# Kernel optimization log

Measured on AMD Instinct MI355X. Metric: run time of the kernel, lower is better.

Reference implementation:

```python
import jax, jax.numpy as jnp
import numpy as np
jax.config.update("jax_enable_x64", True)

N = 16384   # nodes
C = 16      # initial color vocabulary size
B = 64      # number of graphs in the batch
_rs = np.random.RandomState(42)
_MULTS = jnp.asarray((_rs.randint(1, 2 ** 62, size=C + 1).astype(np.int64) << 1) | 1)  # odd 64-bit hash multipliers


def setup_inputs() -> dict:
    key = jax.random.key(0)
    k1, k2, k3 = jax.random.split(key, 3)
    x = jax.random.randint(k1, (N,), 0, C, dtype=jnp.int64)
    adj_t = jax.random.randint(k2, (N, N), 0, 2).astype(jnp.float32)  # dense binary adjacency
    batch = jnp.sort(jax.random.randint(k3, (N,), 0, B, dtype=jnp.int64))
    return {"x": x, "adj_t": adj_t, "batch": batch}


def _wl_colors(x, adj_t):
    # One WL refinement step. The torch code hashes (own_color, sorted neighbor colors)
    # and assigns new ids by insertion order into an OrderedDict ('isolate' -> 0).
    # A sorted tuple of neighbor colors is equivalent to the neighbor color multiset,
    # which we represent as a count histogram and hash with a 64-bit wraparound
    # polynomial hash; ids are then assigned by first-occurrence (node-index) order.
    n = x.shape[0]
    onehot = jax.nn.one_hot(x, C, dtype=adj_t.dtype)                 # [N, C]
    nbr_hist = jnp.round(adj_t @ onehot).astype(jnp.int64)           # [N, C] neighbor color counts
    iso = (adj_t.sum(axis=1) + adj_t.sum(axis=0)) == 0               # isolated nodes
    h = x * _MULTS[0] + (nbr_hist * _MULTS[1:]).sum(axis=-1)         # int64 wraparound hash
    h = jnp.where(iso, jnp.int64(-(2 ** 63)), h)
    order = jnp.argsort(h)
    hs = h[order]
    new_grp = jnp.concatenate([jnp.ones((1,), bool), hs[1:] != hs[:-1]])
    gid = jnp.zeros(n, jnp.int64).at[order].set(jnp.cumsum(new_grp) - 1)   # group id per node
    first_of_grp = jax.ops.segment_min(jnp.arange(n), gid, num_segments=n)
    firsts = first_of_grp[gid]                                       # first node index with same signature
    is_first = (~iso) & (firsts == jnp.arange(n))
    rank = jnp.cumsum(is_first.astype(jnp.int64))                    # hashmap insertion order (1-based)
    return jnp.where(iso, 0, rank[firsts])                           # 'isolate' -> 0


def _histogram(colors, batch):
    # Per-graph color histogram; width padded to N+1 (max possible distinct colors)
    # for static shapes -- extra columns are zero and do not affect the L2 norm.
    num_colors = N + 1
    idx = batch * num_colors + colors
    out = jnp.zeros(B * num_colors, jnp.int64).at[idx].add(1)
    out = out.reshape(B, num_colors)[:, 1:]                          # drop 'isolate' column
    out = out.astype(jnp.float64)
    return out / jnp.linalg.norm(out, axis=-1, keepdims=True)


def reference(x, adj_t, batch):
    colors = _wl_colors(x, adj_t)          # forward's default return value
    hist = _histogram(colors, batch)       # return_embedding=True output
    return hist, colors
```

## Files before the change

### kernel.cpp

```cpp
#include <hip/hip_runtime.h>
#include <stdint.h>

#define NN 16384
#define NC 16
#define NB 64

#define HSIZE 65536
#define HMASK 65535
#define HSENT 0xFFFFFFFFFFFFFFFFull
#define HGOLD 0x9E3779B97F4A7C15ull

typedef unsigned int vuint4 __attribute__((ext_vector_type(4)));

struct Mults { unsigned long long m[17]; };

__device__ __forceinline__ void htab_insert(unsigned long long* __restrict__ hk,
                                            int* __restrict__ hv,
                                            unsigned long long key, int idx) {
  if (key == HSENT) key -= 1;
  unsigned slot = (unsigned)((key * HGOLD) >> 48);
  for (;;) {
    unsigned long long old = atomicCAS(&hk[slot], HSENT, key);
    if (old == HSENT || old == key) { atomicMin(&hv[slot], idx); return; }
    slot = (slot + 1) & HMASK;
  }
}


__global__ __launch_bounds__(256) void k_init(const int* __restrict__ x,
                                              unsigned long long* __restrict__ table,
                                              int* __restrict__ scount,
                                              int* __restrict__ cnt,
                                              unsigned long long* __restrict__ hk,
                                              int* __restrict__ hv) {
  int idx = blockIdx.x * 256 + threadIdx.x;
  if (idx == 0) *scount = 0;
  if (idx < 4096) {
    int c = idx & 15, k = (idx >> 4) & 3, chunk = idx >> 6;
    unsigned long long m = 0ull;
    for (int l = 0; l < 64; ++l) {
      int col = chunk * 256 + l * 4 + k;
      if (x[col] == c) m |= (1ull << l);
    }
    table[idx] = m;
  }
  hk[idx] = HSENT;
  hv[idx] = 0x7fffffff;
  int4 z = {0, 0, 0, 0};
  int4* c4 = (int4*)cnt;
  #pragma unroll
  for (int r = 0; r < 4; ++r) c4[(size_t)idx * 4 + r] = z;
}

__global__ __launch_bounds__(256) void k_hist(const float* __restrict__ adj,
                                              const unsigned long long* __restrict__ table,
                                              const int* __restrict__ x,
                                              Mults M,
                                              unsigned long long* __restrict__ h,
                                              int* __restrict__ iso,
                                              int* __restrict__ suspects,
                                              int* __restrict__ scount,
                                              unsigned long long* __restrict__ hk,
                                              int* __restrict__ hv) {
  int wave = threadIdx.x >> 6;
  int lane = threadIdx.x & 63;
  int row  = blockIdx.x * 4 + wave;
  int xv   = x[row];
  const vuint4* rowp = (const vuint4*)(adj + (size_t)row * NN);
  int c = lane & 15;
  int k = lane >> 4;
  const unsigned long long* tk = table + (k * 16 + c);
  int cnt = 0;
  #pragma unroll 4
  for (int chunk = 0; chunk < 64; ++chunk) {
    vuint4 v = __builtin_nontemporal_load(&rowp[chunk * 64 + lane]);
    unsigned long long tm = tk[chunk * 64];
    unsigned long long b0 = __ballot(v.x != 0u);
    unsigned long long b1 = __ballot(v.y != 0u);
    unsigned long long b2 = __ballot(v.z != 0u);
    unsigned long long b3 = __ballot(v.w != 0u);
    unsigned long long m = (k & 2) ? ((k & 1) ? b3 : b2) : ((k & 1) ? b1 : b0);
    cnt += __popcll(m & tm);
  }
  cnt += __shfl_xor(cnt, 16, 64);
  cnt += __shfl_xor(cnt, 32, 64);
  int rs = cnt;
  rs += __shfl_xor(rs, 1, 64);
  rs += __shfl_xor(rs, 2, 64);
  rs += __shfl_xor(rs, 4, 64);
  rs += __shfl_xor(rs, 8, 64);
  unsigned long long hl = (unsigned long long)(long long)cnt * M.m[(lane & 15) + 1];
  hl += __shfl_xor(hl, 1, 64);
  hl += __shfl_xor(hl, 2, 64);
  hl += __shfl_xor(hl, 4, 64);
  hl += __shfl_xor(hl, 8, 64);
  if (lane == 0) {
    unsigned long long hf = hl + (unsigned long long)(long long)xv * M.m[0];
    h[row] = hf;
    if (rs == 0) {
      int s = atomicAdd(scount, 1);
      suspects[s] = row;
    } else {
      htab_insert(hk, hv, hf, row);
    }
  }
  if (lane == 1) iso[row] = 0;
}

__global__ __launch_bounds__(256) void k_colcheck(const float* __restrict__ adj,
                                                  const int* __restrict__ suspects,
                                                  const int* __restrict__ scount,
                                                  int* __restrict__ iso,
                                                  const unsigned long long* __restrict__ h,
                                                  unsigned long long* __restrict__ hk,
                                                  int* __restrict__ hv) {
  __shared__ int red[256];
  int nsus = *scount;
  for (int u = blockIdx.x; u < nsus; u += gridDim.x) {
    int col = suspects[u];
    int any = 0;
    for (int r = threadIdx.x; r < NN; r += 256)
      any |= (adj[(size_t)r * NN + col] != 0.0f);
    red[threadIdx.x] = any;
    __syncthreads();
    for (int s = 128; s > 0; s >>= 1) {
      if (threadIdx.x < s) red[threadIdx.x] |= red[threadIdx.x + s];
      __syncthreads();
    }
    if (threadIdx.x == 0) {
      if (red[0] == 0) iso[col] = 1;
      else             htab_insert(hk, hv, h[col], col);
    }
    __syncthreads();
  }
}

__global__ __launch_bounds__(256) void k_lookup(const int* __restrict__ iso,
                                                const unsigned long long* __restrict__ h,
                                                const unsigned long long* __restrict__ hk,
                                                const int* __restrict__ hv,
                                                int* __restrict__ firsts) {
  int i = blockIdx.x * 256 + threadIdx.x;
  int f = -1;
  if (!iso[i]) {
    unsigned long long key = h[i];
    if (key == HSENT) key -= 1;
    unsigned slot = (unsigned)((key * HGOLD) >> 48);
    unsigned long long kk = hk[slot];
    while (kk != key) { slot = (slot + 1) & HMASK; kk = hk[slot]; }
    f = hv[slot];
  }
  firsts[i] = f;
}

__global__ __launch_bounds__(1024) void k_scan(const int* __restrict__ firsts,
                                               const int* __restrict__ batch,
                                               float* __restrict__ out_colors,
                                               int* __restrict__ cnt) {
  __shared__ int rank_lds[NN];
  __shared__ int wsum[16];
  int t = threadIdx.x;
  int lane = t & 63, wv = t >> 6;
  int base = t * 16;
  int fidx[16];
  int loc[16];
  int s = 0;
  #pragma unroll
  for (int u = 0; u < 16; ++u) {
    int i = base + u;
    int f = firsts[i];
    fidx[u] = f;
    int isf = (f == i);
    s += isf;
    loc[u] = s;
  }
  int incl = s;
  #pragma unroll
  for (int off = 1; off < 64; off <<= 1) {
    int v = __shfl_up(incl, off, 64);
    if (lane >= off) incl += v;
  }
  if (lane == 63) wsum[wv] = incl;
  __syncthreads();
  if (t == 0) {
    int acc = 0;
    #pragma unroll
    for (int w = 0; w < 16; ++w) { int v = wsum[w]; wsum[w] = acc; acc += v; }
  }
  __syncthreads();
  int excl = wsum[wv] + incl - s;
  #pragma unroll
  for (int u = 0; u < 16; ++u) rank_lds[base + u] = excl + loc[u];
  __syncthreads();
  #pragma unroll
  for (int u = 0; u < 16; ++u) {
    int i = base + u;
    int c = (fidx[u] < 0) ? 0 : rank_lds[fidx[u]];
    out_colors[i] = (float)c;
    if (c > 0) atomicAdd(&cnt[(size_t)batch[i] * NN + (c - 1)], 1);
  }
}

__global__ __launch_bounds__(256) void k_norm(const int* __restrict__ cnt,
                                              float* __restrict__ out) {
  __shared__ float red[256];
  int b = blockIdx.x;
  const int4* c4 = (const int4*)(cnt + (size_t)b * NN);
  float4* o4 = (float4*)(out + (size_t)b * NN);
  float ss = 0.0f;
  for (int j = threadIdx.x; j < NN / 4; j += 256) {
    int4 v = c4[j];
    float4 f = {(float)v.x, (float)v.y, (float)v.z, (float)v.w};
    ss += f.x * f.x + f.y * f.y + f.z * f.z + f.w * f.w;
  }
  red[threadIdx.x] = ss;
  __syncthreads();
  for (int s = 128; s > 0; s >>= 1) {
    if (threadIdx.x < s) red[threadIdx.x] += red[threadIdx.x + s];
    __syncthreads();
  }
  float inv = 1.0f / sqrtf(red[0]);
  for (int j = threadIdx.x; j < NN / 4; j += 256) {
    int4 v = c4[j];
    float4 f = {(float)v.x * inv, (float)v.y * inv, (float)v.z * inv, (float)v.w * inv};
    o4[j] = f;
  }
}


struct MTState { uint32_t mt[624]; int idx; };

static void mt_seed(MTState& s, uint32_t seed) {
  s.mt[0] = seed;
  for (int i = 1; i < 624; ++i)
    s.mt[i] = 1812433253u * (s.mt[i - 1] ^ (s.mt[i - 1] >> 30)) + (uint32_t)i;
  s.idx = 624;
}

static uint32_t mt_next(MTState& s) {
  if (s.idx >= 624) {
    for (int i = 0; i < 624; ++i) {
      uint32_t y = (s.mt[i] & 0x80000000u) | (s.mt[(i + 1) % 624] & 0x7fffffffu);
      uint32_t nx = s.mt[(i + 397) % 624] ^ (y >> 1);
      if (y & 1u) nx ^= 2567483615u;
      s.mt[i] = nx;
    }
    s.idx = 0;
  }
  uint32_t y = s.mt[s.idx++];
  y ^= y >> 11;
  y ^= (y << 7) & 2636928640u;
  y ^= (y << 15) & 4022730752u;
  y ^= y >> 18;
  return y;
}

static uint64_t mt_next64(MTState& s) {
  uint64_t hi = mt_next(s);
  uint64_t lo = mt_next(s);
  return (hi << 32) | lo;
}


extern "C" void kernel_launch(void* const* d_in, const int* in_sizes, int n_in,
                              void* d_out, int out_size, void* d_ws, size_t ws_size,
                              hipStream_t stream) {
  const int*   x     = (const int*)d_in[0];
  const float* adj   = (const float*)d_in[1];
  const int*   batch = (const int*)d_in[2];
  float* out_hist   = (float*)d_out;
  float* out_colors = out_hist + (size_t)NB * NN;

  char* ws = (char*)d_ws;
  int*                cnt      = (int*)(ws + 0);
  int*                scount   = (int*)(ws + 4194304);
  int*                suspects = (int*)(ws + 4194560);
  unsigned long long* h        = (unsigned long long*)(ws + 4260096);
  int*                iso      = (int*)(ws + 4391168);
  int*                firsts   = (int*)(ws + 4456704);
  unsigned long long* table    = (unsigned long long*)(ws + 4522240);
  unsigned long long* hk       = (unsigned long long*)(ws + 4554752);
  int*                hv       = (int*)(ws + 5079040);

  Mults M;
  {
    MTState st;
    mt_seed(st, 42u);
    const uint64_t mask62 = (1ull << 62) - 1ull;
    const uint64_t rng    = (1ull << 62) - 2ull;
    for (int i = 0; i < 17; ++i) {
      uint64_t v;
      do { v = mt_next64(st) & mask62; } while (v > rng);
      M.m[i] = ((1ull + v) << 1) | 1ull;
    }
  }

  k_init<<<256, 256, 0, stream>>>(x, table, scount, cnt, hk, hv);
  k_hist<<<NN / 4, 256, 0, stream>>>(adj, table, x, M, h, iso, suspects, scount, hk, hv);
  k_colcheck<<<64, 256, 0, stream>>>(adj, suspects, scount, iso, h, hk, hv);
  k_lookup<<<NN / 256, 256, 0, stream>>>(iso, h, hk, hv, firsts);
  k_scan<<<1, 1024, 0, stream>>>(firsts, batch, out_colors, cnt);
  k_norm<<<NB, 256, 0, stream>>>(cnt, out_hist);
}
```

Baseline: 1.361 ms.

## Parallelize rank scan, fuse per-graph histogram into LDS, software-pipeline adjacency loads

Measured after the change: 1.343 ms. No clear change (-1.3%).

```diff
diff --git a/kernel.cpp b/kernel.cpp
--- a/kernel.cpp
+++ b/kernel.cpp
@@ -30,7 +30,6 @@
 __global__ __launch_bounds__(256) void k_init(const int* __restrict__ x,
                                               unsigned long long* __restrict__ table,
                                               int* __restrict__ scount,
-                                              int* __restrict__ cnt,
                                               unsigned long long* __restrict__ hk,
                                               int* __restrict__ hv) {
   int idx = blockIdx.x * 256 + threadIdx.x;
@@ -46,11 +45,19 @@
   }
   hk[idx] = HSENT;
   hv[idx] = 0x7fffffff;
-  int4 z = {0, 0, 0, 0};
-  int4* c4 = (int4*)cnt;
-  #pragma unroll
-  for (int r = 0; r < 4; ++r) c4[(size_t)idx * 4 + r] = z;
-}
+}
+
+#define NTLOAD(dv, dt, ch) \
+    dv = __builtin_nontemporal_load(&rowp[(ch) * 64 + lane]); \
+    dt = tkl[(ch) * 64];
+
+#define CONSUME(v, tm) { \
+    unsigned long long b0 = __ballot(v.x != 0u); \
+    unsigned long long b1 = __ballot(v.y != 0u); \
+    unsigned long long b2 = __ballot(v.z != 0u); \
+    unsigned long long b3 = __ballot(v.w != 0u); \
+    unsigned long long m = (k & 2) ? ((k & 1) ? b3 : b2) : ((k & 1) ? b1 : b0); \
+    cnt += __popcll(m & tm); }
 
 __global__ __launch_bounds__(256) void k_hist(const float* __restrict__ adj,
                                               const unsigned long long* __restrict__ table,
@@ -67,21 +74,25 @@
   int row  = blockIdx.x * 4 + wave;
   int xv   = x[row];
   const vuint4* rowp = (const vuint4*)(adj + (size_t)row * NN);
-  int c = lane & 15;
   int k = lane >> 4;
-  const unsigned long long* tk = table + (k * 16 + c);
+  const unsigned long long* tkl = table + lane;
   int cnt = 0;
-  #pragma unroll 4
-  for (int chunk = 0; chunk < 64; ++chunk) {
-    vuint4 v = __builtin_nontemporal_load(&rowp[chunk * 64 + lane]);
-    unsigned long long tm = tk[chunk * 64];
-    unsigned long long b0 = __ballot(v.x != 0u);
-    unsigned long long b1 = __ballot(v.y != 0u);
-    unsigned long long b2 = __ballot(v.z != 0u);
-    unsigned long long b3 = __ballot(v.w != 0u);
-    unsigned long long m = (k & 2) ? ((k & 1) ? b3 : b2) : ((k & 1) ? b1 : b0);
-    cnt += __popcll(m & tm);
-  }
+
+  vuint4 va0, va1, va2, va3, vb0, vb1, vb2, vb3;
+  unsigned long long ta0, ta1, ta2, ta3, tb0, tb1, tb2, tb3;
+  NTLOAD(va0, ta0, 0) NTLOAD(va1, ta1, 1) NTLOAD(va2, ta2, 2) NTLOAD(va3, ta3, 3)
+  #pragma unroll
+  for (int cc = 0; cc < 64; cc += 8) {
+    NTLOAD(vb0, tb0, cc + 4) NTLOAD(vb1, tb1, cc + 5)
+    NTLOAD(vb2, tb2, cc + 6) NTLOAD(vb3, tb3, cc + 7)
+    CONSUME(va0, ta0) CONSUME(va1, ta1) CONSUME(va2, ta2) CONSUME(va3, ta3)
+    if (cc + 8 < 64) {
+      NTLOAD(va0, ta0, cc + 8) NTLOAD(va1, ta1, cc + 9)
+      NTLOAD(va2, ta2, cc + 10) NTLOAD(va3, ta3, cc + 11)
+    }
+    CONSUME(vb0, tb0) CONSUME(vb1, tb1) CONSUME(vb2, tb2) CONSUME(vb3, tb3)
+  }
+
   cnt += __shfl_xor(cnt, 16, 64);
   cnt += __shfl_xor(cnt, 32, 64);
   int rs = cnt;
@@ -139,7 +150,9 @@
                                                 const unsigned long long* __restrict__ h,
                                                 const unsigned long long* __restrict__ hk,
                                                 const int* __restrict__ hv,
-                                                int* __restrict__ firsts) {
+                                                int* __restrict__ firsts,
+                                                int* __restrict__ partial) {
+  __shared__ int red[256];
   int i = blockIdx.x * 256 + threadIdx.x;
   int f = -1;
   if (!iso[i]) {
@@ -151,76 +164,93 @@
     f = hv[slot];
   }
   firsts[i] = f;
-}
-
-__global__ __launch_bounds__(1024) void k_scan(const int* __restrict__ firsts,
-                                               const int* __restrict__ batch,
-                                               float* __restrict__ out_colors,
-                                               int* __restrict__ cnt) {
-  __shared__ int rank_lds[NN];
-  __shared__ int wsum[16];
+  red[threadIdx.x] = (f == i);
+  __syncthreads();
+  for (int s = 128; s > 0; s >>= 1) {
+    if (threadIdx.x < s) red[threadIdx.x] += red[threadIdx.x + s];
+    __syncthreads();
+  }
+  if (threadIdx.x == 0) partial[blockIdx.x] = red[0];
+}
+
+__global__ __launch_bounds__(256) void k_rank(const int* __restrict__ firsts,
+                                              const int* __restrict__ partial,
+                                              int* __restrict__ rank) {
+  __shared__ int wsum[4];
+  __shared__ int sbase;
   int t = threadIdx.x;
   int lane = t & 63, wv = t >> 6;
-  int base = t * 16;
-  int fidx[16];
-  int loc[16];
-  int s = 0;
-  #pragma unroll
-  for (int u = 0; u < 16; ++u) {
-    int i = base + u;
-    int f = firsts[i];
-    fidx[u] = f;
-    int isf = (f == i);
-    s += isf;
-    loc[u] = s;
-  }
-  int incl = s;
+  int i = blockIdx.x * 256 + t;
+  int isf = (firsts[i] == i);
+  int incl = isf;
   #pragma unroll
   for (int off = 1; off < 64; off <<= 1) {
     int v = __shfl_up(incl, off, 64);
     if (lane >= off) incl += v;
   }
   if (lane == 63) wsum[wv] = incl;
-  __syncthreads();
-  if (t == 0) {
-    int acc = 0;
-    #pragma unroll
-    for (int w = 0; w < 16; ++w) { int v = wsum[w]; wsum[w] = acc; acc += v; }
-  }
-  __syncthreads();
-  int excl = wsum[wv] + incl - s;
+  if (t < 64) {
+    int p = (t < blockIdx.x) ? partial[t] : 0;
+    p += __shfl_xor(p, 1, 64);
+    p += __shfl_xor(p, 2, 64);
+    p += __shfl_xor(p, 4, 64);
+    p += __shfl_xor(p, 8, 64);
+    p += __shfl_xor(p, 16, 64);
+    p += __shfl_xor(p, 32, 64);
+    if (t == 0) sbase = p;
+  }
+  __syncthreads();
+  int wbase = 0;
   #pragma unroll
-  for (int u = 0; u < 16; ++u) rank_lds[base + u] = excl + loc[u];
-  __syncthreads();
-  #pragma unroll
-  for (int u = 0; u < 16; ++u) {
-    int i = base + u;
-    int c = (fidx[u] < 0) ? 0 : rank_lds[fidx[u]];
+  for (int w = 0; w < 4; ++w)
+    if (w < wv) wbase += wsum[w];
+  rank[i] = sbase + wbase + incl;
+}
+
+__global__ __launch_bounds__(256) void k_emit_norm(const int* __restrict__ firsts,
+                                                   const int* __restrict__ rank,
+                                                   const int* __restrict__ batch,
+                                                   float* __restrict__ out_colors,
+                                                   float* __restrict__ out) {
+  __shared__ __align__(16) int lhist[NN];
+  __shared__ float red[256];
+  __shared__ int range[2];
+  int b = blockIdx.x;
+  int tid = threadIdx.x;
+  int4* lh4 = (int4*)lhist;
+  int4 z = {0, 0, 0, 0};
+  for (int j = tid; j < NN / 4; j += 256) lh4[j] = z;
+  if (tid < 2) {
+    int target = b + tid;
+    int lo = 0, hi = NN;
+    while (lo < hi) { int mid = (lo + hi) >> 1; if (batch[mid] < target) lo = mid + 1; else hi = mid; }
+    range[tid] = lo;
+  }
+  __syncthreads();
+  int lo = range[0], hi = range[1];
+  for (int i = lo + tid; i < hi; i += 256) {
+    int f = firsts[i];
+    int c = (f < 0) ? 0 : rank[f];
     out_colors[i] = (float)c;
-    if (c > 0) atomicAdd(&cnt[(size_t)batch[i] * NN + (c - 1)], 1);
-  }
-}
-
-__global__ __launch_bounds__(256) void k_norm(const int* __restrict__ cnt,
-                                              float* __restrict__ out) {
-  __shared__ float red[256];
-  int b = blockIdx.x;
-  const int4* c4 = (const int4*)(cnt + (size_t)b * NN);
-  float4* o4 = (float4*)(out + (size_t)b * NN);
+    if (c > 0) atomicAdd(&lhist[c - 1], 1);
+  }
+  __syncthreads();
   float ss = 0.0f;
-  for (int j = threadIdx.x; j < NN / 4; j += 256) {
+  const int4* c4 = (const int4*)lhist;
+  for (int j = tid; j < NN / 4; j += 256) {
     int4 v = c4[j];
     float4 f = {(float)v.x, (float)v.y, (float)v.z, (float)v.w};
     ss += f.x * f.x + f.y * f.y + f.z * f.z + f.w * f.w;
   }
-  red[threadIdx.x] = ss;
+  red[tid] = ss;
   __syncthreads();
   for (int s = 128; s > 0; s >>= 1) {
-    if (threadIdx.x < s) red[threadIdx.x] += red[threadIdx.x + s];
+    if (tid < s) red[tid] += red[tid + s];
     __syncthreads();
   }
   float inv = 1.0f / sqrtf(red[0]);
-  for (int j = threadIdx.x; j < NN / 4; j += 256) {
+  float4* o4 = (float4*)(out + (size_t)b * NN);
+  for (int j = tid; j < NN / 4; j += 256) {
     int4 v = c4[j];
     float4 f = {(float)v.x * inv, (float)v.y * inv, (float)v.z * inv, (float)v.w * inv};
     o4[j] = f;
@@ -272,15 +302,16 @@
   float* out_colors = out_hist + (size_t)NB * NN;
 
   char* ws = (char*)d_ws;
-  int*                cnt      = (int*)(ws + 0);
-  int*                scount   = (int*)(ws + 4194304);
-  int*                suspects = (int*)(ws + 4194560);
-  unsigned long long* h        = (unsigned long long*)(ws + 4260096);
-  int*                iso      = (int*)(ws + 4391168);
-  int*                firsts   = (int*)(ws + 4456704);
-  unsigned long long* table    = (unsigned long long*)(ws + 4522240);
-  unsigned long long* hk       = (unsigned long long*)(ws + 4554752);
-  int*                hv       = (int*)(ws + 5079040);
+  int*                scount   = (int*)(ws + 0);
+  int*                partial  = (int*)(ws + 256);
+  int*                suspects = (int*)(ws + 65536);
+  unsigned long long* h        = (unsigned long long*)(ws + 131072);
+  int*                iso      = (int*)(ws + 262144);
+  int*                firsts   = (int*)(ws + 327680);
+  int*                rank     = (int*)(ws + 393216);
+  unsigned long long* table    = (unsigned long long*)(ws + 458752);
+  unsigned long long* hk       = (unsigned long long*)(ws + 524288);
+  int*                hv       = (int*)(ws + 1048576);
 
   Mults M;
   {
@@ -295,10 +326,10 @@
     }
   }
 
-  k_init<<<256, 256, 0, stream>>>(x, table, scount, cnt, hk, hv);
+  k_init<<<256, 256, 0, stream>>>(x, table, scount, hk, hv);
   k_hist<<<NN / 4, 256, 0, stream>>>(adj, table, x, M, h, iso, suspects, scount, hk, hv);
   k_colcheck<<<64, 256, 0, stream>>>(adj, suspects, scount, iso, h, hk, hv);
-  k_lookup<<<NN / 256, 256, 0, stream>>>(iso, h, hk, hv, firsts);
-  k_scan<<<1, 1024, 0, stream>>>(firsts, batch, out_colors, cnt);
-  k_norm<<<NB, 256, 0, stream>>>(cnt, out_hist);
-}
+  k_lookup<<<NN / 256, 256, 0, stream>>>(iso, h, hk, hv, firsts, partial);
+  k_rank<<<NN / 256, 256, 0, stream>>>(firsts, partial, rank);
+  k_emit_norm<<<NB, 256, 0, stream>>>(firsts, rank, batch, out_colors, out_hist);
+}
```
